# Optimization experiments

Measured on AMD Instinct MI355X. Metric: run time of the kernel, lower is better.

The kernel has to match this reference:

```python
import jax, jax.numpy as jnp
import numpy as np

EMBED = 1024
HEADS = 16
HEAD_DIM = EMBED // HEADS
B, S = 2, 2048


def setup_inputs() -> dict:
    key = jax.random.key(0)
    ks = jax.random.split(key, 9)
    std = 1.0 / np.sqrt(EMBED)
    mk = lambda k: jax.random.uniform(k, (EMBED, EMBED), jnp.float32, -std, std)
    bk = lambda k: jax.random.uniform(k, (EMBED,), jnp.float32, -std, std)
    return {
        "x": jax.random.normal(ks[0], (B, S, EMBED), jnp.float32),
        "Wq": mk(ks[1]), "bq": bk(ks[2]),
        "Wk": mk(ks[3]), "bk": bk(ks[4]),
        "Wv": mk(ks[5]), "bv": bk(ks[6]),
        "Wo": mk(ks[7]), "bo": bk(ks[8]),
    }


def reference(x, Wq, bq, Wk, bk, Wv, bv, Wo, bo):
    b, s, _ = x.shape
    scale = HEAD_DIM ** -0.5
    # Linear layers: y = x @ W^T + b (torch nn.Linear convention)
    def heads(W, bias):
        y = jnp.einsum('bse,fe->bsf', x, W) + bias
        return y.reshape(b, s, HEADS, HEAD_DIM).transpose(0, 2, 1, 3)  # [b,h,s,d]
    Q, K, V = heads(Wq, bq), heads(Wk, bk), heads(Wv, bv)
    scores = jnp.einsum('bhqd,bhkd->bhqk', Q, K) * scale
    attn = jax.nn.softmax(scores, axis=-1)
    out = jnp.einsum('bhqk,bhkd->bhqd', attn, V)
    out = out.transpose(0, 2, 1, 3).reshape(b, s, EMBED)
    return jnp.einsum('bse,fe->bsf', out, Wo) + bo
```

## Files before the change

kernel.cpp:

```cpp
#include <hip/hip_runtime.h>
#include <hip/hip_bf16.h>
#include <cstddef>

#define SEQ   2048
#define EMB   1024
#define NHEAD 16
#define HDIM  64
#define BATCH 2
#define MROWS (BATCH * SEQ)
#define BH_STRIDE (SEQ * HDIM)
#define CSC_F 0.180336874f

typedef __attribute__((ext_vector_type(8))) short frag_ab;
typedef __attribute__((ext_vector_type(4))) float frag_cd;

#define GLOBAL_AS __attribute__((address_space(1)))
#define LDS_AS    __attribute__((address_space(3)))

__device__ __forceinline__ unsigned short f2bf(float f) {
    unsigned u = __float_as_uint(f);
    u += 0x7FFF + ((u >> 16) & 1);
    return (unsigned short)(u >> 16);
}
__device__ __forceinline__ unsigned short f2bf_trunc(float f) {
    return (unsigned short)(__float_as_uint(f) >> 16);
}
__device__ __forceinline__ void gld16(const unsigned short* g, unsigned short* l) {
    __builtin_amdgcn_global_load_lds((GLOBAL_AS const unsigned int*)g,
                                     (LDS_AS unsigned int*)l, 16, 0, 0);
}

__global__ __launch_bounds__(256) void cvt_all(const float* __restrict__ x,
                                               const float* __restrict__ Wq,
                                               const float* __restrict__ Wk,
                                               const float* __restrict__ Wv,
                                               unsigned short* __restrict__ xb,
                                               unsigned short* __restrict__ wqkv) {
    size_t e = ((size_t)blockIdx.x * 256 + threadIdx.x) * 8;
    const float* s;
    unsigned short* d;
    float sc = 1.0f;
    const size_t NX = (size_t)MROWS * EMB;
    const size_t NW = (size_t)EMB * EMB;
    if (e < NX) { s = x + e; d = xb + e; }
    else if (e < NX + NW)     { s = Wq + (e - NX);          d = wqkv + (e - NX); sc = CSC_F; }
    else if (e < NX + 2 * NW) { s = Wk + (e - NX - NW);     d = wqkv + (e - NX); }
    else                      { s = Wv + (e - NX - 2 * NW); d = wqkv + (e - NX); }
    float4 f0 = *(const float4*)s;
    float4 f1 = *(const float4*)(s + 4);
    ushort4 lo, hi;
    lo.x = f2bf(f0.x * sc); lo.y = f2bf(f0.y * sc); lo.z = f2bf(f0.z * sc); lo.w = f2bf(f0.w * sc);
    hi.x = f2bf(f1.x * sc); hi.y = f2bf(f1.y * sc); hi.z = f2bf(f1.z * sc); hi.w = f2bf(f1.w * sc);
    *(ushort4*)d = lo;
    *(ushort4*)(d + 4) = hi;
}

__global__ __launch_bounds__(256) void cvt_bf16(const float* __restrict__ s,
                                                unsigned short* __restrict__ d, int n) {
    int i = (blockIdx.x * 256 + threadIdx.x) * 8;
    if (i >= n) return;
    float4 f0 = *(const float4*)&s[i];
    float4 f1 = *(const float4*)&s[i + 4];
    ushort4 lo, hi;
    lo.x = f2bf(f0.x); lo.y = f2bf(f0.y); lo.z = f2bf(f0.z); lo.w = f2bf(f0.w);
    hi.x = f2bf(f1.x); hi.y = f2bf(f1.y); hi.z = f2bf(f1.z); hi.w = f2bf(f1.w);
    *(ushort4*)&d[i] = lo;
    *(ushort4*)&d[i + 4] = hi;
}

template <bool QKV>
__global__ __launch_bounds__(256, 3) void gemm128(const unsigned short* __restrict__ A,
                                                  const unsigned short* __restrict__ W0,
                                                  const unsigned short* __restrict__ W1,
                                                  const unsigned short* __restrict__ W2,
                                                  const float* __restrict__ b0,
                                                  const float* __restrict__ b1,
                                                  const float* __restrict__ b2,
                                                  void* __restrict__ o0,
                                                  void* __restrict__ o1,
                                                  void* __restrict__ o2) {
    constexpr int K = EMB;
    __shared__ __align__(16) unsigned short SB[16384];
    unsigned short* As = SB;
    unsigned short* Bs = SB + 8192;

    const int bidx = blockIdx.x;
    const int g8 = bidx & 7, t = bidx >> 3;
    const int my = g8 * 4 + (t & 3);
    const int mx = QKV ? ((t >> 2) & 7) : (t >> 2);
    const int z = QKV ? (t >> 5) : 0;

    const unsigned short* W = (z == 0) ? W0 : (z == 1) ? W1 : W2;
    const float* bias = (z == 0) ? b0 : (z == 1) ? b1 : b2;
    void* outv = (z == 0) ? o0 : (z == 1) ? o1 : o2;

    const int m0 = my * 128;
    const int n0 = mx * 128;
    const int tid = threadIdx.x;
    const int lane = tid & 63, w = tid >> 6;
    const int wr = w >> 1, wc = w & 1;
    const int lm = lane & 15, lq = lane >> 4;

    const int cs = (((tid & 7) ^ ((tid >> 3) & 7)) << 3);
    const int sx = lm & 7;

    frag_cd acc[4][4];
#pragma unroll
    for (int mt = 0; mt < 4; ++mt)
#pragma unroll
        for (int nt = 0; nt < 4; ++nt) acc[mt][nt] = (frag_cd){0.f, 0.f, 0.f, 0.f};

    for (int k0 = 0; k0 < K; k0 += 64) {
#pragma unroll
        for (int it = 0; it < 4; ++it) {
            int flat = (it * 256 + tid) * 8;
            int r = flat >> 6;
            gld16(&A[(size_t)(m0 + r) * K + k0 + cs], &As[flat]);
        }
#pragma unroll
        for (int it = 0; it < 4; ++it) {
            int flat = (it * 256 + tid) * 8;
            int r = flat >> 6;
            gld16(&W[(size_t)(n0 + r) * K + k0 + cs], &Bs[flat]);
        }
        __syncthreads();

#pragma unroll
        for (int kk = 0; kk < 2; ++kk) {
            frag_ab af[4], bf[4];
#pragma unroll
            for (int mt = 0; mt < 4; ++mt)
                af[mt] = *(const frag_ab*)&As[(wr * 64 + mt * 16 + lm) * 64
                                              + (((kk * 4 + lq) ^ sx) << 3)];
#pragma unroll
            for (int nt = 0; nt < 4; ++nt)
                bf[nt] = *(const frag_ab*)&Bs[(wc * 64 + nt * 16 + lm) * 64
                                              + (((kk * 4 + lq) ^ sx) << 3)];
#pragma unroll
            for (int mt = 0; mt < 4; ++mt)
#pragma unroll
                for (int nt = 0; nt < 4; ++nt)
                    acc[mt][nt] = __builtin_amdgcn_mfma_f32_16x16x32_bf16(
                        af[mt], bf[nt], acc[mt][nt], 0, 0, 0);
        }
        __syncthreads();
    }

    const float bscale = (QKV && z == 0) ? CSC_F : 1.0f;
    if (!QKV) {
#pragma unroll
        for (int mt = 0; mt < 4; ++mt)
#pragma unroll
            for (int nt = 0; nt < 4; ++nt) {
                int col = n0 + wc * 64 + nt * 16 + lm;
                float bv = bias[col];
#pragma unroll
                for (int r = 0; r < 4; ++r) {
                    int row = m0 + wr * 64 + mt * 16 + lq * 4 + r;
                    ((float*)outv)[(size_t)row * EMB + col] = acc[mt][nt][r] + bv;
                }
            }
    } else {
#pragma unroll
        for (int mt = 0; mt < 4; ++mt)
#pragma unroll
            for (int nt = 0; nt < 4; ++nt) {
                int col = n0 + wc * 64 + nt * 16 + lm;
                float bv = bias[col] * bscale;
#pragma unroll
                for (int r = 0; r < 4; ++r) {
                    unsigned short o = f2bf(acc[mt][nt][r] + bv);
                    int l, pos;
                    if (z < 2) {
                        l = wc * 16 + (wr * 4 + mt) * 2 + (nt >> 1);
                        pos = ((nt * 2 + (lm >> 3)) & 3) * 128 + (lq * 4 + r) * 8 + (lm & 7);
                    } else {
                        l = wc * 16 + (wr * 2 + (mt >> 1)) * 4 + nt;
                        pos = ((mt & 1) * 2 + (lq >> 1)) * 128 + lm * 8 + (lq & 1) * 4 + r;
                    }
                    SB[l * 512 + pos] = o;
                }
            }
        __syncthreads();

        unsigned short* out = (unsigned short*)outv;
        const int b = m0 >> 11;
        const int hb = n0 >> 6;
        const int sg16 = (m0 & (SEQ - 1)) >> 4;
        const int sb32 = (m0 & (SEQ - 1)) >> 5;
#pragma unroll
        for (int it = 0; it < 8; ++it) {
            int cl = it * 4 + w;
            uint4 v = *(const uint4*)&SB[cl * 512 + lane * 8];
            size_t chunk;
            if (z < 2) {
                int h = cl >> 4, sg = (cl >> 1) & 7, dh = cl & 1;
                chunk = ((size_t)(b * NHEAD + hb + h) * 128 + sg16 + sg) * 2 + dh;
            } else {
                int h = cl >> 4, sb = (cl >> 2) & 3, dq = cl & 3;
                chunk = ((size_t)(b * NHEAD + hb + h) * 64 + sb32 + sb) * 4 + dq;
            }
            *(uint4*)&out[chunk * 512 + lane * 8] = v;
        }
    }
}

#define PSTRIDE 72
#define CSTRIDE 81

__global__ __launch_bounds__(256, 2) void attn_fused(const unsigned short* __restrict__ Q,
                                                     const unsigned short* __restrict__ Kf,
                                                     const unsigned short* __restrict__ Vf,
                                                     unsigned short* __restrict__ O) {
    const int bidx = blockIdx.x;
    const int g8 = bidx & 7, t = bidx >> 3;
    const int bh = g8 * 4 + (t & 3);
    const int qt = t >> 2;
    const int w = threadIdx.x >> 6, lane = threadIdx.x & 63;
    const int lm = lane & 15, lq = lane >> 4;
    const int qs = w & 1;
    const int kh = w >> 1;

    __shared__ __align__(16) unsigned char SMEM[2 * 64 * CSTRIDE * 4 * sizeof(float) / 4];
    unsigned short* P = (unsigned short*)SMEM;

    const unsigned short* Qb = Q + (size_t)bh * BH_STRIDE;
    const unsigned short* Kb = Kf + (size_t)bh * BH_STRIDE;
    const unsigned short* Vb = Vf + (size_t)bh * BH_STRIDE;

    const int ga = qt * 8 + qs * 4;
    frag_ab qf[4][2];
#pragma unroll
    for (int qi = 0; qi < 4; ++qi) {
        qf[qi][0] = *(const frag_ab*)&Qb[(((ga + qi) * 2 + 0) * 64 + lane) * 8];
        qf[qi][1] = *(const frag_ab*)&Qb[(((ga + qi) * 2 + 1) * 64 + lane) * 8];
    }

    frag_ab vone;
#pragma unroll
    for (int j = 0; j < 8; ++j) vone[j] = (short)0x3F80;

    frag_cd oa[4][4], oc[4];
#pragma unroll
    for (int qi = 0; qi < 4; ++qi) {
        oc[qi] = (frag_cd){0.f, 0.f, 0.f, 0.f};
#pragma unroll
        for (int dt = 0; dt < 4; ++dt) oa[qi][dt] = (frag_cd){0.f, 0.f, 0.f, 0.f};
    }

    unsigned short* Pw = &P[w * (64 * PSTRIDE)];
    const frag_cd z = (frag_cd){0.f, 0.f, 0.f, 0.f};

    const int j_base = kh * (SEQ / 2);
    for (int jj = 0; jj < SEQ / 2; jj += 64) {
        const int j = j_base + jj;
        const int kg = j >> 4, jb = j >> 5;

        frag_ab kc[4][2], vc[2][4];
#pragma unroll
        for (int c = 0; c < 4; ++c) {
            kc[c][0] = *(const frag_ab*)&Kb[(((kg + c) * 2 + 0) * 64 + lane) * 8];
            kc[c][1] = *(const frag_ab*)&Kb[(((kg + c) * 2 + 1) * 64 + lane) * 8];
        }
#pragma unroll
        for (int j2 = 0; j2 < 2; ++j2)
#pragma unroll
            for (int dt = 0; dt < 4; ++dt)
                vc[j2][dt] = *(const frag_ab*)&Vb[(((jb + j2) * 4 + dt) * 64 + lane) * 8];

#pragma unroll
        for (int c = 0; c < 4; ++c) {
#pragma unroll
            for (int qi = 0; qi < 4; ++qi) {
                frag_cd sc = __builtin_amdgcn_mfma_f32_16x16x32_bf16(qf[qi][0], kc[c][0], z, 0, 0, 0);
                sc = __builtin_amdgcn_mfma_f32_16x16x32_bf16(qf[qi][1], kc[c][1], sc, 0, 0, 0);
#pragma unroll
                for (int r = 0; r < 4; ++r) {
                    float p = __builtin_amdgcn_exp2f(sc[r]);
                    Pw[(qi * 16 + lq * 4 + r) * PSTRIDE + c * 16 + lm] = f2bf_trunc(p);
                }
            }
        }

#pragma unroll
        for (int qi = 0; qi < 4; ++qi) {
            frag_ab pf0 = *(const frag_ab*)&Pw[(qi * 16 + lm) * PSTRIDE + lq * 8];
            frag_ab pf1 = *(const frag_ab*)&Pw[(qi * 16 + lm) * PSTRIDE + 32 + lq * 8];
            oc[qi] = __builtin_amdgcn_mfma_f32_16x16x32_bf16(pf0, vone, oc[qi], 0, 0, 0);
            oc[qi] = __builtin_amdgcn_mfma_f32_16x16x32_bf16(pf1, vone, oc[qi], 0, 0, 0);
#pragma unroll
            for (int dt = 0; dt < 4; ++dt) {
                oa[qi][dt] = __builtin_amdgcn_mfma_f32_16x16x32_bf16(pf0, vc[0][dt], oa[qi][dt], 0, 0, 0);
                oa[qi][dt] = __builtin_amdgcn_mfma_f32_16x16x32_bf16(pf1, vc[1][dt], oa[qi][dt], 0, 0, 0);
            }
        }
    }

    __syncthreads();
    float* C = (float*)SMEM;
    if (w >= 2) {
        float* dst = C + (size_t)(w - 2) * (64 * CSTRIDE) + lane * CSTRIDE;
        int idx = 0;
#pragma unroll
        for (int qi = 0; qi < 4; ++qi)
#pragma unroll
            for (int dt = 0; dt < 4; ++dt)
#pragma unroll
                for (int r = 0; r < 4; ++r) dst[idx++] = oa[qi][dt][r];
#pragma unroll
        for (int qi = 0; qi < 4; ++qi)
#pragma unroll
            for (int r = 0; r < 4; ++r) dst[idx++] = oc[qi][r];
    }
    __syncthreads();
    if (w < 2) {
        const float* src = C + (size_t)w * (64 * CSTRIDE) + lane * CSTRIDE;
        int idx = 0;
#pragma unroll
        for (int qi = 0; qi < 4; ++qi)
#pragma unroll
            for (int dt = 0; dt < 4; ++dt)
#pragma unroll
                for (int r = 0; r < 4; ++r) oa[qi][dt][r] += src[idx++];
#pragma unroll
        for (int qi = 0; qi < 4; ++qi)
#pragma unroll
            for (int r = 0; r < 4; ++r) oc[qi][r] += src[idx++];

        const int b = bh >> 4, h = bh & (NHEAD - 1);
#pragma unroll
        for (int qi = 0; qi < 4; ++qi) {
            const int q0 = (ga + qi) * 16;
#pragma unroll
            for (int r = 0; r < 4; ++r) {
                float inv = 1.0f / oc[qi][r];
                int srow = q0 + lq * 4 + r;
#pragma unroll
                for (int dt = 0; dt < 4; ++dt) {
                    int d = dt * 16 + lm;
                    O[((size_t)(b * SEQ + srow)) * EMB + h * HDIM + d] = f2bf(oa[qi][dt][r] * inv);
                }
            }
        }
    }
}

extern "C" void kernel_launch(void* const* d_in, const int* in_sizes, int n_in,
                              void* d_out, int out_size, void* d_ws, size_t ws_size,
                              hipStream_t stream) {
    const float* x  = (const float*)d_in[0];
    const float* Wq = (const float*)d_in[1];
    const float* bq = (const float*)d_in[2];
    const float* Wk = (const float*)d_in[3];
    const float* bk = (const float*)d_in[4];
    const float* Wv = (const float*)d_in[5];
    const float* bv = (const float*)d_in[6];
    const float* Wo = (const float*)d_in[7];
    const float* bo = (const float*)d_in[8];

    unsigned short* xb    = (unsigned short*)d_ws;
    unsigned short* q_ws  = xb + (size_t)MROWS * EMB;
    unsigned short* k_ws  = q_ws + (size_t)MROWS * EMB;
    unsigned short* vt_ws = k_ws + (size_t)MROWS * EMB;
    unsigned short* o_ws  = xb;
    unsigned short* wqkv  = (unsigned short*)d_out;
    unsigned short* wo_b  = q_ws;

    dim3 blk(256);
    cvt_all<<<dim3((MROWS * EMB + 3 * EMB * EMB) / 2048), blk, 0, stream>>>(
        x, Wq, Wk, Wv, xb, wqkv);

    gemm128<true><<<dim3(768), blk, 0, stream>>>(
        xb, wqkv, wqkv + EMB * EMB, wqkv + 2 * EMB * EMB,
        bq, bk, bv, q_ws, k_ws, vt_ws);

    attn_fused<<<dim3(512), blk, 0, stream>>>(q_ws, k_ws, vt_ws, o_ws);

    cvt_bf16<<<dim3(EMB * EMB / 2048), blk, 0, stream>>>(Wo, wo_b, EMB * EMB);
    gemm128<false><<<dim3(256), blk, 0, stream>>>(
        o_ws, wo_b, wo_b, wo_b, bo, bo, bo, d_out, d_out, d_out);
}
```

Baseline: 179.9 us.

## Split attention KV range across four waves per query tile, double grid

```diff
diff --git a/kernel.cpp b/kernel.cpp
--- a/kernel.cpp
+++ b/kernel.cpp
@@ -206,9 +206,8 @@
 }
 
 #define PSTRIDE 72
-#define CSTRIDE 81
-
-__global__ __launch_bounds__(256, 2) void attn_fused(const unsigned short* __restrict__ Q,
+
+__global__ __launch_bounds__(256, 4) void attn_fused(const unsigned short* __restrict__ Q,
                                                      const unsigned short* __restrict__ Kf,
                                                      const unsigned short* __restrict__ Vf,
                                                      unsigned short* __restrict__ O) {
@@ -218,17 +217,15 @@
     const int qt = t >> 2;
     const int w = threadIdx.x >> 6, lane = threadIdx.x & 63;
     const int lm = lane & 15, lq = lane >> 4;
-    const int qs = w & 1;
-    const int kh = w >> 1;
-
-    __shared__ __align__(16) unsigned char SMEM[2 * 64 * CSTRIDE * 4 * sizeof(float) / 4];
+
+    __shared__ __align__(16) unsigned char SMEM[40960];
     unsigned short* P = (unsigned short*)SMEM;
 
     const unsigned short* Qb = Q + (size_t)bh * BH_STRIDE;
     const unsigned short* Kb = Kf + (size_t)bh * BH_STRIDE;
     const unsigned short* Vb = Vf + (size_t)bh * BH_STRIDE;
 
-    const int ga = qt * 8 + qs * 4;
+    const int ga = qt * 4;
     frag_ab qf[4][2];
 #pragma unroll
     for (int qi = 0; qi < 4; ++qi) {
@@ -251,8 +248,8 @@
     unsigned short* Pw = &P[w * (64 * PSTRIDE)];
     const frag_cd z = (frag_cd){0.f, 0.f, 0.f, 0.f};
 
-    const int j_base = kh * (SEQ / 2);
-    for (int jj = 0; jj < SEQ / 2; jj += 64) {
+    const int j_base = w * (SEQ / 4);
+    for (int jj = 0; jj < SEQ / 4; jj += 64) {
         const int j = j_base + jj;
         const int kg = j >> 4, jb = j >> 5;
 
@@ -296,36 +293,67 @@
         }
     }
 
+    float* C = (float*)SMEM;
+    float* R0 = C;
+    float* R1 = C + 5120;
+
     __syncthreads();
-    float* C = (float*)SMEM;
     if (w >= 2) {
-        float* dst = C + (size_t)(w - 2) * (64 * CSTRIDE) + lane * CSTRIDE;
+        float* dst = (w == 2) ? R0 : R1;
         int idx = 0;
 #pragma unroll
         for (int qi = 0; qi < 4; ++qi)
 #pragma unroll
             for (int dt = 0; dt < 4; ++dt)
 #pragma unroll
-                for (int r = 0; r < 4; ++r) dst[idx++] = oa[qi][dt][r];
-#pragma unroll
-        for (int qi = 0; qi < 4; ++qi)
-#pragma unroll
-            for (int r = 0; r < 4; ++r) dst[idx++] = oc[qi][r];
+                for (int r = 0; r < 4; ++r) { dst[idx * 64 + lane] = oa[qi][dt][r]; ++idx; }
+#pragma unroll
+        for (int qi = 0; qi < 4; ++qi)
+#pragma unroll
+            for (int r = 0; r < 4; ++r) { dst[idx * 64 + lane] = oc[qi][r]; ++idx; }
     }
     __syncthreads();
     if (w < 2) {
-        const float* src = C + (size_t)w * (64 * CSTRIDE) + lane * CSTRIDE;
+        const float* src = (w == 0) ? R0 : R1;
         int idx = 0;
 #pragma unroll
         for (int qi = 0; qi < 4; ++qi)
 #pragma unroll
             for (int dt = 0; dt < 4; ++dt)
 #pragma unroll
-                for (int r = 0; r < 4; ++r) oa[qi][dt][r] += src[idx++];
-#pragma unroll
-        for (int qi = 0; qi < 4; ++qi)
-#pragma unroll
-            for (int r = 0; r < 4; ++r) oc[qi][r] += src[idx++];
+                for (int r = 0; r < 4; ++r) { oa[qi][dt][r] += src[idx * 64 + lane]; ++idx; }
+#pragma unroll
+        for (int qi = 0; qi < 4; ++qi)
+#pragma unroll
+            for (int r = 0; r < 4; ++r) { oc[qi][r] += src[idx * 64 + lane]; ++idx; }
+    }
+    __syncthreads();
+    if (w == 1) {
+        int idx = 0;
+#pragma unroll
+        for (int qi = 0; qi < 4; ++qi)
+#pragma unroll
+            for (int dt = 0; dt < 4; ++dt)
+#pragma unroll
+                for (int r = 0; r < 4; ++r) { R0[idx * 64 + lane] = oa[qi][dt][r]; ++idx; }
+#pragma unroll
+        for (int qi = 0; qi < 4; ++qi)
+#pragma unroll
+            for (int r = 0; r < 4; ++r) { R0[idx * 64 + lane] = oc[qi][r]; ++idx; }
+    }
+    __syncthreads();
+    if (w == 0) {
+        int idx = 0;
+#pragma unroll
+        for (int qi = 0; qi < 4; ++qi)
+#pragma unroll
+            for (int dt = 0; dt < 4; ++dt)
+#pragma unroll
+                for (int r = 0; r < 4; ++r) { oa[qi][dt][r] += R0[idx * 64 + lane]; ++idx; }
+#pragma unroll
+        for (int qi = 0; qi < 4; ++qi)
+#pragma unroll
+            for (int r = 0; r < 4; ++r) { oc[qi][r] += R0[idx * 64 + lane]; ++idx; }
 
         const int b = bh >> 4, h = bh & (NHEAD - 1);
 #pragma unroll
@@ -374,7 +402,7 @@
         xb, wqkv, wqkv + EMB * EMB, wqkv + 2 * EMB * EMB,
         bq, bk, bv, q_ws, k_ws, vt_ws);
 
-    attn_fused<<<dim3(512), blk, 0, stream>>>(q_ws, k_ws, vt_ws, o_ws);
+    attn_fused<<<dim3(1024), blk, 0, stream>>>(q_ws, k_ws, vt_ws, o_ws);
 
     cvt_bf16<<<dim3(EMB * EMB / 2048), blk, 0, stream>>>(Wo, wo_b, EMB * EMB);
     gemm128<false><<<dim3(256), blk, 0, stream>>>(
```

Result: slower. 332.1 us (+84.5%).
